# Optimization experiments

Hardware: AMD Instinct MI355X
Metric: run time of the kernel (lower is better)

The kernel has to match this reference:

```python
import jax, jax.numpy as jnp
import numpy as np

ROOT_2 = 1.41421
C = 256
DIV = 4
CP = C // DIV  # 64


def _spectral_normalize(w2d):
    # exact largest singular value (torch uses power iteration approx of this)
    s = jnp.linalg.norm(w2d, ord=2)
    return w2d / s


def setup_inputs() -> dict:
    key = jax.random.key(0)
    ks = jax.random.split(key, 10)
    B, H, W = 8, 64, 64
    x = jax.random.normal(ks[0], (B, C, H, W), dtype=jnp.float32)
    # 1x1 conv weights stored as [out, in]; spectral-normalized like torch's spectral_norm
    def conv_w(k, o, i):
        w = jax.random.normal(k, (o, i), dtype=jnp.float32) * (1.0 / np.sqrt(i))
        return _spectral_normalize(w)
    Wq = conv_w(ks[1], CP, C); bq = jnp.zeros((CP,), jnp.float32)
    Wk = conv_w(ks[2], CP, C); bk = jnp.zeros((CP,), jnp.float32)
    Wv = conv_w(ks[3], CP, C); bv = jnp.zeros((CP,), jnp.float32)
    Wo = conv_w(ks[4], C, CP); bo = jnp.zeros((C,), jnp.float32)
    gamma = jnp.zeros((1,), jnp.float32)
    return {"x": x, "Wq": Wq, "bq": bq, "Wk": Wk, "bk": bk,
            "Wv": Wv, "bv": bv, "Wo": Wo, "bo": bo, "gamma": gamma}


def reference(x, Wq, bq, Wk, bk, Wv, bv, Wo, bo, gamma):
    B, c, h, w = x.shape
    n = h * w
    const1 = jnp.float32(ROOT_2 / np.sqrt(C))       # Weight_Scaling(in_channels)
    const2 = jnp.float32(ROOT_2 / np.sqrt(CP))      # Weight_Scaling(in_channels//div_num)
    xs = (const1 * x).reshape(B, c, n)              # [B,C,N]
    q = jnp.einsum('oc,bcn->bon', Wq, xs) + bq[None, :, None]  # [B,C',N]
    k = jnp.einsum('oc,bcn->bon', Wk, xs) + bk[None, :, None]
    v = jnp.einsum('oc,bcn->bon', Wv, xs) + bv[None, :, None]
    # attn[b,i,j] = softmax_j(q[:,i]^T k[:,j])
    scores = jnp.einsum('bcn,bcm->bnm', q, k)       # [B,N,N]
    attn = jax.nn.softmax(scores, axis=-1)
    sa = jnp.einsum('bcm,bnm->bcn', v, attn)        # v @ attn^T
    sa = const2 * sa
    out = jnp.einsum('oc,bcn->bon', Wo, sa) + bo[None, :, None]  # [B,C,N]
    out = out.reshape(B, c, h, w)
    return gamma[0] * out + x
```

## Files before the change

kernel.cpp:

```cpp
#include <hip/hip_runtime.h>


#define Bsz 8
#define Cch 256
#define CPd 64
#define Nn  4096
#define TIL 64
#define NSPL 2
#define MHALF (Nn / NSPL)

typedef __attribute__((ext_vector_type(8))) short short8;
typedef __attribute__((ext_vector_type(4))) float f32x4;

static constexpr float C1 = (float)(1.41421 / 16.0);
static constexpr float C2 = (float)(1.41421 / 8.0);

__device__ inline unsigned pk_trunc(float lo, float hi) {
    return __builtin_amdgcn_perm(__float_as_uint(hi), __float_as_uint(lo), 0x07060302u);
}
__device__ inline float dpp_swap1(float v) {
    return __uint_as_float((unsigned)__builtin_amdgcn_mov_dpp(
        (int)__float_as_uint(v), 0xB1, 0xF, 0xF, true));
}

__global__ __launch_bounds__(256) void wconv_kernel(
    const float* __restrict__ Wq, const float* __restrict__ Wk,
    const float* __restrict__ Wv, const float* __restrict__ Wo,
    unsigned short* __restrict__ Wb)
{
    const int idx = (blockIdx.x * 256 + threadIdx.x) * 4;
    const float* src = (idx < 16384) ? Wq : (idx < 32768) ? Wk : (idx < 49152) ? Wv : Wo;
    const float4 v = *(const float4*)(src + (idx & 16383));
    *(uint2*)(Wb + idx) = make_uint2(pk_trunc(v.x, v.y), pk_trunc(v.z, v.w));
}

__global__ __launch_bounds__(256) void qkv_kernel(
    const float* __restrict__ x, const unsigned short* __restrict__ Wb,
    const float* __restrict__ bq, const float* __restrict__ bk, const float* __restrict__ bv,
    unsigned short* __restrict__ qT, unsigned short* __restrict__ kT,
    unsigned short* __restrict__ vB)
{
    __shared__ __align__(16) unsigned short Wlds[CPd * 264];
    __shared__ __align__(16) float T[TIL * 68];

    const int b   = blockIdx.y;
    const int n0  = blockIdx.x * TIL;
    const int t   = threadIdx.x;
    const int g   = t >> 6;
    const int l15 = t & 15;
    const int l4  = (t & 63) >> 4;

    const float* xb = x + (size_t)b * Cch * Nn + n0 + 16 * g + l15;
    short8 xf[8];
    #pragma unroll
    for (int ks = 0; ks < 8; ++ks) {
        float xr[8];
        #pragma unroll
        for (int j = 0; j < 8; ++j)
            xr[j] = C1 * xb[(size_t)(8 * l4 + 32 * ks + j) * Nn];
        union { unsigned u[4]; short8 s; } p;
        p.u[0] = pk_trunc(xr[0], xr[1]); p.u[1] = pk_trunc(xr[2], xr[3]);
        p.u[2] = pk_trunc(xr[4], xr[5]); p.u[3] = pk_trunc(xr[6], xr[7]);
        xf[ks] = p.s;
    }

    #pragma unroll
    for (int mat = 0; mat < 3; ++mat) {
        {
            const uint4* wg = (const uint4*)(Wb + mat * 16384);
            #pragma unroll
            for (int p = 0; p < 8; ++p) {
                const int idx = p * 256 + t;
                const int o = idx >> 5, cs = idx & 31;
                *(uint4*)&Wlds[o * 264 + cs * 8] = wg[idx];
            }
        }
        __syncthreads();

        const float* bias = (mat == 0) ? bq : (mat == 1) ? bk : bv;
        f32x4 acc[4];
        #pragma unroll
        for (int st = 0; st < 4; ++st) {
            const float bb = bias[16 * st + l15];
            acc[st] = (f32x4){bb, bb, bb, bb};
        }
        #pragma unroll
        for (int st = 0; st < 4; ++st) {
            #pragma unroll
            for (int ks = 0; ks < 8; ++ks) {
                const short8 wf = *(const short8*)&Wlds[(16 * st + l15) * 264 + 8 * l4 + 32 * ks];
                acc[st] = __builtin_amdgcn_mfma_f32_16x16x32_bf16(xf[ks], wf, acc[st], 0, 0, 0);
            }
        }
        __syncthreads();

        if (mat < 2) {
            #pragma unroll
            for (int st = 0; st < 4; ++st)
                #pragma unroll
                for (int r = 0; r < 4; ++r)
                    T[(16 * g + 4 * l4 + r) * 68 + 16 * st + l15] = acc[st][r];
        } else {
            #pragma unroll
            for (int st = 0; st < 4; ++st)
                #pragma unroll
                for (int r = 0; r < 4; ++r)
                    T[(16 * st + l15) * 68 + 16 * g + 4 * l4 + r] = acc[st][r];
        }
        __syncthreads();

        const int row = t >> 2;
        const int sg  = 16 * (t & 3);
        const float4 a0 = *(const float4*)&T[row * 68 + sg + 0];
        const float4 a1 = *(const float4*)&T[row * 68 + sg + 4];
        const float4 a2 = *(const float4*)&T[row * 68 + sg + 8];
        const float4 a3 = *(const float4*)&T[row * 68 + sg + 12];
        const uint4 lo = make_uint4(pk_trunc(a0.x, a0.y), pk_trunc(a0.z, a0.w),
                                    pk_trunc(a1.x, a1.y), pk_trunc(a1.z, a1.w));
        const uint4 hi = make_uint4(pk_trunc(a2.x, a2.y), pk_trunc(a2.z, a2.w),
                                    pk_trunc(a3.x, a3.y), pk_trunc(a3.z, a3.w));
        unsigned short* dst;
        if (mat < 2) {
            dst = (mat == 0 ? qT : kT) + ((size_t)(b * Nn + n0 + row)) * CPd + sg;
        } else {
            dst = vB + ((size_t)(b * CPd + row)) * Nn + n0 + sg;
        }
        *(uint4*)dst = lo;
        *(uint4*)(dst + 8) = hi;
    }
}

__global__ __launch_bounds__(256, 4) void flash_kernel(
    const unsigned short* __restrict__ qT, const unsigned short* __restrict__ kT,
    const unsigned short* __restrict__ vB, float* __restrict__ Op, float* __restrict__ Lg)
{
    __shared__ __align__(16) unsigned short Ks[TIL * 72];
    __shared__ __align__(16) unsigned short Vs[TIL * 72];
    __shared__ __align__(16) unsigned Pb[TIL * 36];
    __shared__ float Lsh[TIL];

    const int b   = blockIdx.y;
    const int n0  = blockIdx.x * TIL;
    const int s   = blockIdx.z;
    const int t   = threadIdx.x;
    const int l   = t & 63;
    const int g   = t >> 6;
    const int l15 = l & 15;
    const int l4  = l >> 4;
    const int par = l & 1;
    const unsigned sel = par ? 0x03020706u : 0x07060302u;
    const int l15h = l15 >> 1;

    if (t < TIL) Lsh[t] = 0.f;

    const unsigned short* qp = qT + (size_t)(b * Nn + n0 + 16 * g + l15) * CPd + 8 * l4;
    const short8 qf0 = *(const short8*)qp;
    const short8 qf1 = *(const short8*)(qp + 32);

    f32x4 acco[4];
    #pragma unroll
    for (int ct = 0; ct < 4; ++ct) acco[ct] = (f32x4){0.f, 0.f, 0.f, 0.f};
    float Lp[4] = {0.f, 0.f, 0.f, 0.f};

    const uint4* kg = (const uint4*)(kT + (size_t)b * Nn * CPd);
    const unsigned short* vb = vB + (size_t)b * CPd * Nn;
    const int mbase = s * MHALF;

    for (int mi = 0; mi < MHALF; mi += TIL) {
        const int m0 = mbase + mi;
        __syncthreads();
        {
            const int r = t >> 3, cc = t & 7;
            uint4 k0 = kg[(m0 + r) * 8 + cc];
            uint4 k1 = kg[(m0 + r + 32) * 8 + cc];
            *(uint4*)&Ks[r * 72 + 8 * cc]        = k0;
            *(uint4*)&Ks[(r + 32) * 72 + 8 * cc] = k1;
            uint4 w0 = *(const uint4*)(vb + (size_t)r * Nn + m0 + 8 * cc);
            uint4 w1 = *(const uint4*)(vb + (size_t)(r + 32) * Nn + m0 + 8 * cc);
            *(uint4*)&Vs[r * 72 + 8 * cc]        = w0;
            *(uint4*)&Vs[(r + 32) * 72 + 8 * cc] = w1;
        }
        __syncthreads();

        f32x4 accs[4];
        #pragma unroll
        for (int st = 0; st < 4; ++st) {
            accs[st] = (f32x4){0.f, 0.f, 0.f, 0.f};
            const short8 kf0 = *(const short8*)&Ks[(16 * st + l15) * 72 + 8 * l4];
            const short8 kf1 = *(const short8*)&Ks[(16 * st + l15) * 72 + 8 * l4 + 32];
            accs[st] = __builtin_amdgcn_mfma_f32_16x16x32_bf16(qf0, kf0, accs[st], 0, 0, 0);
            accs[st] = __builtin_amdgcn_mfma_f32_16x16x32_bf16(qf1, kf1, accs[st], 0, 0, 0);
        }

        #pragma unroll
        for (int st = 0; st < 4; ++st) {
            unsigned u[4];
            #pragma unroll
            for (int r = 0; r < 4; ++r) {
                float p = __expf(accs[st][r]);
                Lp[r] += p;
                float nb = dpp_swap1(p);
                u[r] = __builtin_amdgcn_perm(__float_as_uint(nb), __float_as_uint(p), sel);
            }
            const int rb = 16 * g + 4 * l4 + 2 * par;
            Pb[(rb + 0) * 36 + 8 * st + l15h] = u[2 * par];
            Pb[(rb + 1) * 36 + 8 * st + l15h] = u[2 * par + 1];
        }
        __syncthreads();

        #pragma unroll
        for (int ks = 0; ks < 2; ++ks) {
            const short8 pf = *(const short8*)&Pb[(16 * g + l15) * 36 + 4 * l4 + 16 * ks];
            #pragma unroll
            for (int ct = 0; ct < 4; ++ct) {
                const short8 vf = *(const short8*)&Vs[(16 * ct + l15) * 72 + 8 * l4 + 32 * ks];
                acco[ct] = __builtin_amdgcn_mfma_f32_16x16x32_bf16(pf, vf, acco[ct], 0, 0, 0);
            }
        }
    }

    #pragma unroll
    for (int r = 0; r < 4; ++r) atomicAdd(&Lsh[16 * g + 4 * l4 + r], Lp[r]);
    __syncthreads();

    float* ob = Op + ((size_t)(s * Bsz + b) * Nn + n0) * CPd;
    #pragma unroll
    for (int r = 0; r < 4; ++r) {
        const int nl = 16 * g + 4 * l4 + r;
        #pragma unroll
        for (int ct = 0; ct < 4; ++ct)
            ob[(size_t)nl * CPd + 16 * ct + l15] = acco[ct][r];
    }
    if (t < TIL) Lg[(size_t)(s * Bsz + b) * Nn + n0 + t] = Lsh[t];
}

__global__ __launch_bounds__(512) void out_kernel(
    const float* __restrict__ Op, const float* __restrict__ Lg,
    const unsigned short* __restrict__ Wob,
    const float* __restrict__ bo, const float* __restrict__ gamma,
    const float* __restrict__ x, float* __restrict__ y)
{
    __shared__ __align__(16) unsigned short Wos[Cch * 72];
    __shared__ __align__(16) unsigned short Sas[TIL * 72];
    __shared__ float bos[Cch];

    const int b   = blockIdx.y;
    const int n0  = blockIdx.x * TIL;
    const int t   = threadIdx.x;
    const int l   = t & 63;
    const int w   = t >> 6;
    const int l15 = l & 15;
    const int l4  = l >> 4;

    if (t < Cch) bos[t] = bo[t];
    {
        const uint4* wg = (const uint4*)Wob;
        #pragma unroll
        for (int p = 0; p < 4; ++p) {
            const int idx = p * 512 + t;
            const int row = idx >> 3, seg = idx & 7;
            *(uint4*)&Wos[row * 72 + seg * 8] = wg[idx];
        }
    }
    if (t < 256) {
        const int n = t >> 2, seg = t & 3;
        const float* o0 = Op + ((size_t)(b * Nn + n0 + n)) * CPd + seg * 16;
        const float* o1 = o0 + (size_t)Bsz * Nn * CPd;
        const float l0 = Lg[(size_t)b * Nn + n0 + n];
        const float l1 = Lg[(size_t)(Bsz + b) * Nn + n0 + n];
        const float sc = C2 / (l0 + l1);
        unsigned pk[8];
        #pragma unroll
        for (int i = 0; i < 4; ++i) {
            const float4 a = ((const float4*)o0)[i];
            const float4 c = ((const float4*)o1)[i];
            pk[2 * i]     = pk_trunc((a.x + c.x) * sc, (a.y + c.y) * sc);
            pk[2 * i + 1] = pk_trunc((a.z + c.z) * sc, (a.w + c.w) * sc);
        }
        *(uint4*)&Sas[n * 72 + seg * 16]     = make_uint4(pk[0], pk[1], pk[2], pk[3]);
        *(uint4*)&Sas[n * 72 + seg * 16 + 8] = make_uint4(pk[4], pk[5], pk[6], pk[7]);
    }
    __syncthreads();

    short8 bfr[4][2];
    #pragma unroll
    for (int ns = 0; ns < 4; ++ns) {
        bfr[ns][0] = *(const short8*)&Sas[(16 * ns + l15) * 72 + 8 * l4];
        bfr[ns][1] = *(const short8*)&Sas[(16 * ns + l15) * 72 + 8 * l4 + 32];
    }
    const float gam = gamma[0];
    const float* xb = x + (size_t)b * Cch * Nn;
    float*       yb = y + (size_t)b * Cch * Nn;

    #pragma unroll
    for (int os2 = 0; os2 < 2; ++os2) {
        const int obase = 16 * (w + 8 * os2);
        const short8 af0 = *(const short8*)&Wos[(obase + l15) * 72 + 8 * l4];
        const short8 af1 = *(const short8*)&Wos[(obase + l15) * 72 + 8 * l4 + 32];
        #pragma unroll
        for (int ns = 0; ns < 4; ++ns) {
            f32x4 acc = (f32x4){0.f, 0.f, 0.f, 0.f};
            acc = __builtin_amdgcn_mfma_f32_16x16x32_bf16(af0, bfr[ns][0], acc, 0, 0, 0);
            acc = __builtin_amdgcn_mfma_f32_16x16x32_bf16(af1, bfr[ns][1], acc, 0, 0, 0);
            #pragma unroll
            for (int r = 0; r < 4; ++r) {
                const int o = obase + 4 * l4 + r;
                const size_t idx = (size_t)o * Nn + n0 + 16 * ns + l15;
                yb[idx] = fmaf(gam, acc[r] + bos[o], xb[idx]);
            }
        }
    }
}

extern "C" void kernel_launch(void* const* d_in, const int* in_sizes, int n_in,
                              void* d_out, int out_size, void* d_ws, size_t ws_size,
                              hipStream_t stream)
{
    (void)in_sizes; (void)n_in; (void)out_size; (void)ws_size;
    const float* x     = (const float*)d_in[0];
    const float* Wq    = (const float*)d_in[1];
    const float* bq    = (const float*)d_in[2];
    const float* Wk    = (const float*)d_in[3];
    const float* bk    = (const float*)d_in[4];
    const float* Wv    = (const float*)d_in[5];
    const float* bv    = (const float*)d_in[6];
    const float* Wo    = (const float*)d_in[7];
    const float* bo    = (const float*)d_in[8];
    const float* gamma = (const float*)d_in[9];
    float* y = (float*)d_out;

    const size_t per = (size_t)Bsz * Nn * CPd;
    unsigned short* qT = (unsigned short*)d_ws;
    unsigned short* kT = qT + per;
    unsigned short* vB = kT + per;
    float* Op = (float*)(vB + per);
    float* Lg = Op + NSPL * per;
    unsigned short* Wb = (unsigned short*)(Lg + NSPL * Bsz * Nn);

    dim3 grid(Nn / TIL, Bsz);
    dim3 gridF(Nn / TIL, Bsz, NSPL);
    wconv_kernel<<<64, 256, 0, stream>>>(Wq, Wk, Wv, Wo, Wb);
    qkv_kernel<<<grid, 256, 0, stream>>>(x, Wb, bq, bk, bv, qT, kT, vB);
    flash_kernel<<<gridF, 256, 0, stream>>>(qT, kT, vB, Op, Lg);
    out_kernel<<<grid, 512, 0, stream>>>(Op, Lg, Wb + 3 * 16384, bo, gamma, x, y);
}
```

Measured before the change: 189.8 us.

## Split KV four ways, load tiles via global_load_lds with XOR swizzle, atomic-reduce partials

The flash kernel now splits the key range into four chunks instead of two and raises the occupancy hint. K/V tiles are copied straight from global memory into LDS with global_load_lds, using an XOR-swizzled, unpadded layout in place of staging through registers into padded rows. Partial outputs and row sums are combined with float atomics into a single buffer that is zeroed by a memset, so the output kernel reads one partial instead of two. This adds atomic traffic, makes the summation order nondeterministic, and adds a memset launch.

```diff
diff --git a/kernel.cpp b/kernel.cpp
--- a/kernel.cpp
+++ b/kernel.cpp
@@ -6,8 +6,8 @@
 #define CPd 64
 #define Nn  4096
 #define TIL 64
-#define NSPL 2
-#define MHALF (Nn / NSPL)
+#define NSPL 4
+#define MQUAR (Nn / NSPL)
 
 typedef __attribute__((ext_vector_type(8))) short short8;
 typedef __attribute__((ext_vector_type(4))) float f32x4;
@@ -21,6 +21,11 @@
 __device__ inline float dpp_swap1(float v) {
     return __uint_as_float((unsigned)__builtin_amdgcn_mov_dpp(
         (int)__float_as_uint(v), 0xB1, 0xF, 0xF, true));
+}
+__device__ __forceinline__ void gl16(const unsigned short* g, unsigned short* s) {
+    __builtin_amdgcn_global_load_lds(
+        (const __attribute__((address_space(1))) void*)g,
+        (__attribute__((address_space(3))) void*)s, 16, 0, 0);
 }
 
 __global__ __launch_bounds__(256) void wconv_kernel(
@@ -130,13 +135,13 @@
     }
 }
 
-__global__ __launch_bounds__(256, 4) void flash_kernel(
+__global__ __launch_bounds__(256, 6) void flash_kernel(
     const unsigned short* __restrict__ qT, const unsigned short* __restrict__ kT,
     const unsigned short* __restrict__ vB, float* __restrict__ Op, float* __restrict__ Lg)
 {
-    __shared__ __align__(16) unsigned short Ks[TIL * 72];
-    __shared__ __align__(16) unsigned short Vs[TIL * 72];
-    __shared__ __align__(16) unsigned Pb[TIL * 36];
+    __shared__ __align__(16) unsigned short Ks[TIL * 64];
+    __shared__ __align__(16) unsigned short Vs[TIL * 64];
+    __shared__ __align__(16) unsigned Pb[TIL * 34];
     __shared__ float Lsh[TIL];
 
     const int b   = blockIdx.y;
@@ -162,32 +167,36 @@
     for (int ct = 0; ct < 4; ++ct) acco[ct] = (f32x4){0.f, 0.f, 0.f, 0.f};
     float Lp[4] = {0.f, 0.f, 0.f, 0.f};
 
-    const uint4* kg = (const uint4*)(kT + (size_t)b * Nn * CPd);
-    const unsigned short* vb = vB + (size_t)b * CPd * Nn;
-    const int mbase = s * MHALF;
-
-    for (int mi = 0; mi < MHALF; mi += TIL) {
+    const int r16 = (l >> 3) & 7;
+    const int sch = (l & 7) ^ r16;
+    const unsigned short* kSrc = kT + (size_t)b * Nn * CPd
+                               + (size_t)(16 * g + r16) * CPd + sch * 8;
+    const unsigned short* vSrc = vB + (size_t)b * CPd * Nn
+                               + (size_t)(16 * g + r16) * Nn + sch * 8;
+    unsigned short* KsW = &Ks[(16 * g) * 64];
+    unsigned short* VsW = &Vs[(16 * g) * 64];
+
+    const int h7  = l15 & 7;
+    const int sw0 = (l4 ^ h7) << 4;
+    const char* KsB = (const char*)Ks + (l15 << 7);
+    const char* VsB = (const char*)Vs + (l15 << 7);
+
+    const int mbase = s * MQUAR;
+    for (int mi = 0; mi < MQUAR; mi += TIL) {
         const int m0 = mbase + mi;
         __syncthreads();
-        {
-            const int r = t >> 3, cc = t & 7;
-            uint4 k0 = kg[(m0 + r) * 8 + cc];
-            uint4 k1 = kg[(m0 + r + 32) * 8 + cc];
-            *(uint4*)&Ks[r * 72 + 8 * cc]        = k0;
-            *(uint4*)&Ks[(r + 32) * 72 + 8 * cc] = k1;
-            uint4 w0 = *(const uint4*)(vb + (size_t)r * Nn + m0 + 8 * cc);
-            uint4 w1 = *(const uint4*)(vb + (size_t)(r + 32) * Nn + m0 + 8 * cc);
-            *(uint4*)&Vs[r * 72 + 8 * cc]        = w0;
-            *(uint4*)&Vs[(r + 32) * 72 + 8 * cc] = w1;
-        }
+        gl16(kSrc + (size_t)m0 * CPd,       KsW);
+        gl16(kSrc + (size_t)(m0 + 8) * CPd, KsW + 8 * 64);
+        gl16(vSrc + m0,                     VsW);
+        gl16(vSrc + (size_t)8 * Nn + m0,    VsW + 8 * 64);
         __syncthreads();
 
         f32x4 accs[4];
         #pragma unroll
         for (int st = 0; st < 4; ++st) {
             accs[st] = (f32x4){0.f, 0.f, 0.f, 0.f};
-            const short8 kf0 = *(const short8*)&Ks[(16 * st + l15) * 72 + 8 * l4];
-            const short8 kf1 = *(const short8*)&Ks[(16 * st + l15) * 72 + 8 * l4 + 32];
+            const short8 kf0 = *(const short8*)(KsB + (st << 11) + sw0);
+            const short8 kf1 = *(const short8*)(KsB + (st << 11) + (sw0 ^ 64));
             accs[st] = __builtin_amdgcn_mfma_f32_16x16x32_bf16(qf0, kf0, accs[st], 0, 0, 0);
             accs[st] = __builtin_amdgcn_mfma_f32_16x16x32_bf16(qf1, kf1, accs[st], 0, 0, 0);
         }
@@ -203,17 +212,18 @@
                 u[r] = __builtin_amdgcn_perm(__float_as_uint(nb), __float_as_uint(p), sel);
             }
             const int rb = 16 * g + 4 * l4 + 2 * par;
-            Pb[(rb + 0) * 36 + 8 * st + l15h] = u[2 * par];
-            Pb[(rb + 1) * 36 + 8 * st + l15h] = u[2 * par + 1];
+            Pb[(rb + 0) * 34 + 8 * st + l15h] = u[2 * par];
+            Pb[(rb + 1) * 34 + 8 * st + l15h] = u[2 * par + 1];
         }
         __syncthreads();
 
         #pragma unroll
         for (int ks = 0; ks < 2; ++ks) {
-            const short8 pf = *(const short8*)&Pb[(16 * g + l15) * 36 + 4 * l4 + 16 * ks];
+            const short8 pf = *(const short8*)&Pb[(16 * g + l15) * 34 + 4 * l4 + 16 * ks];
+            const int swk = sw0 ^ (ks << 6);
             #pragma unroll
             for (int ct = 0; ct < 4; ++ct) {
-                const short8 vf = *(const short8*)&Vs[(16 * ct + l15) * 72 + 8 * l4 + 32 * ks];
+                const short8 vf = *(const short8*)(VsB + (ct << 11) + swk);
                 acco[ct] = __builtin_amdgcn_mfma_f32_16x16x32_bf16(pf, vf, acco[ct], 0, 0, 0);
             }
         }
@@ -223,15 +233,15 @@
     for (int r = 0; r < 4; ++r) atomicAdd(&Lsh[16 * g + 4 * l4 + r], Lp[r]);
     __syncthreads();
 
-    float* ob = Op + ((size_t)(s * Bsz + b) * Nn + n0) * CPd;
+    float* ob = Op + ((size_t)(b * Nn + n0)) * CPd;
     #pragma unroll
     for (int r = 0; r < 4; ++r) {
         const int nl = 16 * g + 4 * l4 + r;
         #pragma unroll
         for (int ct = 0; ct < 4; ++ct)
-            ob[(size_t)nl * CPd + 16 * ct + l15] = acco[ct][r];
-    }
-    if (t < TIL) Lg[(size_t)(s * Bsz + b) * Nn + n0 + t] = Lsh[t];
+            atomicAdd(&ob[(size_t)nl * CPd + 16 * ct + l15], acco[ct][r]);
+    }
+    if (t < TIL) atomicAdd(&Lg[(size_t)b * Nn + n0 + t], Lsh[t]);
 }
 
 __global__ __launch_bounds__(512) void out_kernel(
@@ -265,17 +275,13 @@
     if (t < 256) {
         const int n = t >> 2, seg = t & 3;
         const float* o0 = Op + ((size_t)(b * Nn + n0 + n)) * CPd + seg * 16;
-        const float* o1 = o0 + (size_t)Bsz * Nn * CPd;
-        const float l0 = Lg[(size_t)b * Nn + n0 + n];
-        const float l1 = Lg[(size_t)(Bsz + b) * Nn + n0 + n];
-        const float sc = C2 / (l0 + l1);
+        const float sc = C2 / Lg[(size_t)b * Nn + n0 + n];
         unsigned pk[8];
         #pragma unroll
         for (int i = 0; i < 4; ++i) {
             const float4 a = ((const float4*)o0)[i];
-            const float4 c = ((const float4*)o1)[i];
-            pk[2 * i]     = pk_trunc((a.x + c.x) * sc, (a.y + c.y) * sc);
-            pk[2 * i + 1] = pk_trunc((a.z + c.z) * sc, (a.w + c.w) * sc);
+            pk[2 * i]     = pk_trunc(a.x * sc, a.y * sc);
+            pk[2 * i + 1] = pk_trunc(a.z * sc, a.w * sc);
         }
         *(uint4*)&Sas[n * 72 + seg * 16]     = make_uint4(pk[0], pk[1], pk[2], pk[3]);
         *(uint4*)&Sas[n * 72 + seg * 16 + 8] = make_uint4(pk[4], pk[5], pk[6], pk[7]);
@@ -334,8 +340,10 @@
     unsigned short* kT = qT + per;
     unsigned short* vB = kT + per;
     float* Op = (float*)(vB + per);
-    float* Lg = Op + NSPL * per;
-    unsigned short* Wb = (unsigned short*)(Lg + NSPL * Bsz * Nn);
+    float* Lg = Op + per;
+    unsigned short* Wb = (unsigned short*)(Lg + (size_t)Bsz * Nn);
+
+    hipMemsetAsync(Op, 0, (per + (size_t)Bsz * Nn) * sizeof(float), stream);
 
     dim3 grid(Nn / TIL, Bsz);
     dim3 gridF(Nn / TIL, Bsz, NSPL);
```

New measurement: 190.8 us. Within noise of the previous version (+0.5%).
